# Kernel optimization log

Measured on AMD Instinct MI355X. Metric: run time of the kernel, lower is better.

Reference implementation:

```python
import jax, jax.numpy as jnp
import numpy as np

N_HEAD = 16
D_HEAD = 64
SCALE = 1.0 / D_HEAD ** 0.5


def setup_inputs() -> dict:
    key = jax.random.key(0)
    k1, k2, k3, k4 = jax.random.split(key, 4)
    bsz, qlen, d_embed, d_model = 4, 1024, 768, 1024
    return {
        "word_emb": jax.random.normal(k1, (bsz, qlen, d_embed), dtype=jnp.float32),
        "emb_w": jax.random.normal(k2, (d_embed, d_model), dtype=jnp.float32) * 0.02,
        "emb_b": jnp.zeros((d_model,), dtype=jnp.float32),
        "qkv_w0": jax.random.normal(k3, (d_model, 3 * N_HEAD * D_HEAD), dtype=jnp.float32) * 0.02,
        "qkv_w1": jax.random.normal(k4, (d_model, 3 * N_HEAD * D_HEAD), dtype=jnp.float32) * 0.02,
    }


def _mha(h, qkv_w):
    # h: [qlen, bsz, d_model]
    qlen, bsz, _ = h.shape
    heads = h @ qkv_w  # [qlen, bsz, 3*n_head*d_head]
    head_q, head_k, head_v = jnp.split(heads, 3, axis=-1)
    head_q = head_q.reshape(qlen, bsz, N_HEAD, D_HEAD)
    head_k = head_k.reshape(qlen, bsz, N_HEAD, D_HEAD)
    head_v = head_v.reshape(qlen, bsz, N_HEAD, D_HEAD)
    # explicit score materialization, faithful to the source einsum pattern
    attn_score = jnp.einsum('ibnd,jbnd->ijbn', head_q, head_k) * SCALE
    attn_prob = jax.nn.softmax(attn_score, axis=1)  # softmax over klen (dim=1)
    attn_vec = jnp.einsum('ijbn,jbnd->ibnd', attn_prob, head_v)
    attn_vec = attn_vec.reshape(qlen, bsz, N_HEAD * D_HEAD)
    return attn_vec, attn_prob


def reference(word_emb, emb_w, emb_b, qkv_w0, qkv_w1):
    # word_emb: [bsz, qlen, d_embed] -> [qlen, bsz, d_embed]
    h = jnp.transpose(word_emb, (1, 0, 2))
    h = h @ emb_w + emb_b  # emb_proj since d_embed != d_model
    # NOTE: the source computes pos_emb and word_emb + pos_emb, but then
    # overwrites with core_out = self.drop(word_emb), discarding pos_emb.
    # Dropout is identity in reference (eval) mode, so core_out == h.
    core_out = h
    core_out, attn_maps = _mha(core_out, qkv_w0)
    core_out, attn_maps = _mha(core_out, qkv_w1)
    return core_out, attn_maps
```

## Files before the change

### kernel.cpp

```cpp
#include <hip/hip_runtime.h>

#define LOG2E 1.44269504088896340736f

typedef __attribute__((ext_vector_type(8))) short short8;
typedef __attribute__((ext_vector_type(4))) short short4v;
typedef __attribute__((ext_vector_type(4))) float floatx4;

__device__ __forceinline__ float bf2f(short s) {
    union { float f; unsigned u; } v; v.u = ((unsigned)(unsigned short)s) << 16; return v.f;
}
__device__ __forceinline__ short f2bf(float f) {
    union { float f; unsigned u; } v; v.f = f;
    unsigned u = v.u;
    u += 0x7FFFu + ((u >> 16) & 1u);
    return (short)(u >> 16);
}

__device__ __forceinline__ void gl_lds16(const void* g, void* l) {
    __builtin_amdgcn_global_load_lds((const __attribute__((address_space(1))) void*)g,
                                     (__attribute__((address_space(3))) void*)l, 16, 0, 0);
}

__global__ __launch_bounds__(256) void wcast(const float* __restrict__ W,
                                             short* __restrict__ Wt, int K, int N) {
    __shared__ float tile[64][65];
    int n0 = blockIdx.x * 64, k0 = blockIdx.y * 64;
    int t = threadIdx.x;
    int r = t >> 2, c4 = (t & 3) * 16;
    const float* src = W + (size_t)(k0 + r) * N + n0 + c4;
#pragma unroll
    for (int q = 0; q < 16; ++q) tile[r][c4 + q] = src[q];
    __syncthreads();
    short* dst = Wt + (size_t)(n0 + r) * K + k0 + c4;
    short8 o1, o2;
#pragma unroll
    for (int q = 0; q < 8; ++q) o1[q] = f2bf(tile[c4 + q][r]);
#pragma unroll
    for (int q = 0; q < 8; ++q) o2[q] = f2bf(tile[c4 + 8 + q][r]);
    *(short8*)(dst) = o1;
    *(short8*)(dst + 8) = o2;
}

__global__ __launch_bounds__(256) void a0cast(const float* __restrict__ we,
                                              short* __restrict__ A0) {
    int e = blockIdx.x * 256 + threadIdx.x;
    int m = e / 96, dc = (e % 96) * 8;
    int b = m & 3, s = m >> 2;
    const float* src = we + (size_t)(b * 1024 + s) * 768 + dc;
    short8 o;
#pragma unroll
    for (int q = 0; q < 8; ++q) o[q] = f2bf(src[q]);
    *(short8*)(A0 + (size_t)m * 768 + dc) = o;
}

__global__ __launch_bounds__(256) void gemm_bt(const short* __restrict__ A,
                                               const short* __restrict__ Bt,
                                               short* __restrict__ C,
                                               const float* __restrict__ bias,
                                               int K, int N) {
    __shared__ __align__(16) short sA[128 * 32];
    __shared__ __align__(16) short sB[128 * 32];
    int n0 = blockIdx.x * 128, m0 = blockIdx.y * 128;
    int tid = threadIdx.x;
    int lane = tid & 63, w = tid >> 6;
    int wm = (w >> 1) * 64, wn = (w & 1) * 64;
    int l15 = lane & 15, quad = lane >> 4;
    int srow = lane >> 2, scoff = (lane & 3) * 8;

    floatx4 zero = {0.f, 0.f, 0.f, 0.f};
    floatx4 acc[4][4];
#pragma unroll
    for (int i = 0; i < 4; ++i)
#pragma unroll
        for (int j = 0; j < 4; ++j) acc[i][j] = zero;

    for (int k0 = 0; k0 < K; k0 += 32) {
#pragma unroll
        for (int h = 0; h < 2; ++h) {
            int seg = w * 2 + h;
            int row = seg * 16 + srow;
            gl_lds16(A + (size_t)(m0 + row) * K + k0 + scoff, sA + seg * 512);
            gl_lds16(Bt + (size_t)(n0 + row) * K + k0 + scoff, sB + seg * 512);
        }
        __syncthreads();
        short8 af[4], bfr[4];
#pragma unroll
        for (int i = 0; i < 4; ++i) {
            af[i]  = *(const short8*)(sA + (wm + i * 16 + l15) * 32 + quad * 8);
            bfr[i] = *(const short8*)(sB + (wn + i * 16 + l15) * 32 + quad * 8);
        }
#pragma unroll
        for (int i = 0; i < 4; ++i)
#pragma unroll
            for (int j = 0; j < 4; ++j)
                acc[i][j] = __builtin_amdgcn_mfma_f32_16x16x32_bf16(af[i], bfr[j], acc[i][j], 0, 0, 0);
        __syncthreads();
    }
#pragma unroll
    for (int i = 0; i < 4; ++i)
#pragma unroll
        for (int j = 0; j < 4; ++j) {
            int col = n0 + wn + j * 16 + l15;
            float bv = bias ? bias[col] : 0.f;
#pragma unroll
            for (int r = 0; r < 4; ++r) {
                int row = m0 + wm + i * 16 + quad * 4 + r;
                C[(size_t)row * N + col] = f2bf(acc[i][j][r] + bv);
            }
        }
}

__global__ __launch_bounds__(256) void pack_qkv(const short* __restrict__ heads,
                                                short* __restrict__ Qp,
                                                short* __restrict__ Kp,
                                                short* __restrict__ Vtp) {
    __shared__ short vt[64][72];
    int bn = blockIdx.y;
    int b = bn >> 4, n = bn & 15;
    int j0 = blockIdx.x * 64;
    int t = threadIdx.x;
#pragma unroll
    for (int h = 0; h < 2; ++h) {
        int c = t + h * 256;
        int jj = c >> 3, off = (c & 7) * 8;
        const short* base = heads + (size_t)((j0 + jj) * 4 + b) * 3072 + n * 64 + off;
        short8 qv = *(const short8*)(base);
        short8 kv = *(const short8*)(base + 1024);
        short8 vv = *(const short8*)(base + 2048);
        short8 qs;
#pragma unroll
        for (int e = 0; e < 8; ++e) qs[e] = f2bf(bf2f(qv[e]) * 0.125f);
        *(short8*)(Qp + (size_t)bn * 65536 + (j0 + jj) * 64 + off) = qs;
        *(short8*)(Kp + (size_t)bn * 65536 + (j0 + jj) * 64 + off) = kv;
#pragma unroll
        for (int e = 0; e < 8; ++e) vt[jj][off + e] = vv[e];
    }
    __syncthreads();
#pragma unroll
    for (int h = 0; h < 2; ++h) {
        int c = t + h * 256;
        int d = c >> 3, joff = (c & 7) * 8;
        short8 o;
#pragma unroll
        for (int e = 0; e < 8; ++e) o[e] = vt[joff + e][d];
        *(short8*)(Vtp + (size_t)bn * 65536 + d * 1024 + j0 + joff) = o;
    }
}

template <bool L2>
__global__ __launch_bounds__(64) void fattn(const short* __restrict__ Qp,
                                            const short* __restrict__ Kp,
                                            const short* __restrict__ Vtp,
                                            void* __restrict__ Optr,
                                            float* __restrict__ linv) {
    __shared__ __align__(16) short plds[32 * 32];
    int bn = blockIdx.y, b = bn >> 4, n = bn & 15;
    int i0 = blockIdx.x * 32;
    int lane = threadIdx.x, l15 = lane & 15, quad = lane >> 4;
    const short* Qb = Qp + (size_t)bn * 65536;
    const short* Kb = Kp + (size_t)bn * 65536;
    const short* Vb = Vtp + (size_t)bn * 65536;

    short8 qf[2][2];
#pragma unroll
    for (int ib = 0; ib < 2; ++ib) {
        qf[ib][0] = *(const short8*)(Qb + (i0 + ib * 16 + l15) * 64 + quad * 8);
        qf[ib][1] = *(const short8*)(Qb + (i0 + ib * 16 + l15) * 64 + 32 + quad * 8);
    }
    floatx4 zero = {0.f, 0.f, 0.f, 0.f};
    floatx4 o[2][4];
#pragma unroll
    for (int ib = 0; ib < 2; ++ib)
#pragma unroll
        for (int tt = 0; tt < 4; ++tt) o[ib][tt] = zero;
    float lsum[2] = {0.f, 0.f};

    for (int j0 = 0; j0 < 1024; j0 += 32) {
#pragma unroll
        for (int jb = 0; jb < 2; ++jb) {
            const short* kr = Kb + (j0 + jb * 16 + l15) * 64 + quad * 8;
            short8 kf0 = *(const short8*)(kr);
            short8 kf1 = *(const short8*)(kr + 32);
#pragma unroll
            for (int ib = 0; ib < 2; ++ib) {
                floatx4 s = zero;
                s = __builtin_amdgcn_mfma_f32_16x16x32_bf16(kf0, qf[ib][0], s, 0, 0, 0);
                s = __builtin_amdgcn_mfma_f32_16x16x32_bf16(kf1, qf[ib][1], s, 0, 0, 0);
                short4v pk;
                float ls = 0.f;
#pragma unroll
                for (int r = 0; r < 4; ++r) {
                    float p = __builtin_amdgcn_exp2f(s[r] * LOG2E);
                    ls += p;
                    pk[r] = f2bf(p);
                }
                lsum[ib] += ls;
                *(short4v*)(plds + (ib * 16 + l15) * 32 + jb * 16 + quad * 4) = pk;
            }
        }
        __syncthreads();
        short8 pa[2];
        pa[0] = *(const short8*)(plds + l15 * 32 + quad * 8);
        pa[1] = *(const short8*)(plds + (16 + l15) * 32 + quad * 8);
#pragma unroll
        for (int tt = 0; tt < 4; ++tt) {
            short8 vf = *(const short8*)(Vb + (tt * 16 + l15) * 1024 + j0 + quad * 8);
#pragma unroll
            for (int ib = 0; ib < 2; ++ib)
                o[ib][tt] = __builtin_amdgcn_mfma_f32_16x16x32_bf16(pa[ib], vf, o[ib][tt], 0, 0, 0);
        }
        __syncthreads();
    }
    float rinv[2];
#pragma unroll
    for (int ib = 0; ib < 2; ++ib) {
        float t = lsum[ib];
        t += __shfl_xor(t, 16);
        t += __shfl_xor(t, 32);
        rinv[ib] = 1.f / t;
    }
    if (L2 && quad == 0) {
        linv[bn * 1024 + i0 + l15] = rinv[0];
        linv[bn * 1024 + i0 + 16 + l15] = rinv[1];
    }
    float rn[2][4];
#pragma unroll
    for (int ib = 0; ib < 2; ++ib)
#pragma unroll
        for (int r = 0; r < 4; ++r)
            rn[ib][r] = __shfl(rinv[ib], quad * 4 + r);
#pragma unroll
    for (int ib = 0; ib < 2; ++ib)
#pragma unroll
        for (int tt = 0; tt < 4; ++tt)
#pragma unroll
            for (int r = 0; r < 4; ++r) {
                float val = o[ib][tt][r] * rn[ib][r];
                int row = i0 + ib * 16 + quad * 4 + r;
                int col = n * 64 + tt * 16 + l15;
                size_t idx = (size_t)(row * 4 + b) * 1024 + col;
                if (L2) ((float*)Optr)[idx] = val;
                else    ((short*)Optr)[idx] = f2bf(val);
            }
}

__global__ __launch_bounds__(256) void pfin(const short* __restrict__ Qp,
                                            const short* __restrict__ Kp,
                                            const float* __restrict__ linv,
                                            float* __restrict__ Pout) {
    __shared__ short sP[64 * 512];
    int j0 = blockIdx.x * 32, i0 = blockIdx.y * 16;
    int tid = threadIdx.x, wv = tid >> 6, lane = tid & 63;
    int l15 = lane & 15, quad = lane >> 4;
    floatx4 zero = {0.f, 0.f, 0.f, 0.f};
    for (int bi = 0; bi < 16; ++bi) {
        int bn = wv * 16 + bi;
        const short* Qb = Qp + (size_t)bn * 65536;
        const short* Kb = Kp + (size_t)bn * 65536;
        short8 qf0 = *(const short8*)(Qb + (i0 + l15) * 64 + quad * 8);
        short8 qf1 = *(const short8*)(Qb + (i0 + l15) * 64 + 32 + quad * 8);
        float li = linv[bn * 1024 + i0 + l15];
#pragma unroll
        for (int jb = 0; jb < 2; ++jb) {
            const short* kr = Kb + (j0 + jb * 16 + l15) * 64 + quad * 8;
            short8 kf0 = *(const short8*)(kr);
            short8 kf1 = *(const short8*)(kr + 32);
            floatx4 s = zero;
            s = __builtin_amdgcn_mfma_f32_16x16x32_bf16(kf0, qf0, s, 0, 0, 0);
            s = __builtin_amdgcn_mfma_f32_16x16x32_bf16(kf1, qf1, s, 0, 0, 0);
            short4v pk;
#pragma unroll
            for (int r = 0; r < 4; ++r)
                pk[r] = f2bf(__builtin_amdgcn_exp2f(s[r] * LOG2E) * li);
            *(short4v*)(sP + bn * 512 + l15 * 32 + jb * 16 + quad * 4) = pk;
        }
    }
    __syncthreads();
    int ii = tid >> 4, q = tid & 15;
    float* dst = Pout + (size_t)(i0 + ii) * 65536 + j0 * 64 + q * 128;
#pragma unroll
    for (int e4 = 0; e4 < 32; ++e4) {
        int pos = q * 128 + e4 * 4;
        int jj = pos >> 6, bnb = pos & 63;
        float4 v;
        v.x = bf2f(sP[(bnb + 0) * 512 + ii * 32 + jj]);
        v.y = bf2f(sP[(bnb + 1) * 512 + ii * 32 + jj]);
        v.z = bf2f(sP[(bnb + 2) * 512 + ii * 32 + jj]);
        v.w = bf2f(sP[(bnb + 3) * 512 + ii * 32 + jj]);
        *(float4*)(dst + e4 * 4) = v;
    }
}

extern "C" void kernel_launch(void* const* d_in, const int* in_sizes, int n_in,
                              void* d_out, int out_size, void* d_ws, size_t ws_size,
                              hipStream_t stream) {
    const float* word_emb = (const float*)d_in[0];
    const float* emb_w    = (const float*)d_in[1];
    const float* emb_b    = (const float*)d_in[2];
    const float* qkv_w0   = (const float*)d_in[3];
    const float* qkv_w1   = (const float*)d_in[4];
    float* out0 = (float*)d_out;
    float* out1 = out0 + 4194304;

    char* ws = (char*)d_ws;
    short* A0    = (short*)(ws);
    short* WtE   = (short*)(ws + 6291456);
    short* Wt0   = (short*)(ws + 7864320);
    short* Wt1   = (short*)(ws + 14155776);
    short* hbuf  = (short*)(ws + 20447232);
    short* h2    = (short*)(ws + 28835840);
    short* heads = (short*)(ws + 37224448);
    short* Qp    = (short*)(ws + 62390272);
    short* Kp    = (short*)(ws + 70778880);
    short* Vtp   = (short*)(ws + 79167488);
    float* linv  = (float*)(ws + 87556096);

    wcast<<<dim3(16, 12), 256, 0, stream>>>(emb_w, WtE, 768, 1024);
    wcast<<<dim3(48, 16), 256, 0, stream>>>(qkv_w0, Wt0, 1024, 3072);
    wcast<<<dim3(48, 16), 256, 0, stream>>>(qkv_w1, Wt1, 1024, 3072);
    a0cast<<<1536, 256, 0, stream>>>(word_emb, A0);

    gemm_bt<<<dim3(8, 32), 256, 0, stream>>>(A0, WtE, hbuf, emb_b, 768, 1024);
    gemm_bt<<<dim3(24, 32), 256, 0, stream>>>(hbuf, Wt0, heads, nullptr, 1024, 3072);
    pack_qkv<<<dim3(16, 64), 256, 0, stream>>>(heads, Qp, Kp, Vtp);
    fattn<false><<<dim3(32, 64), 64, 0, stream>>>(Qp, Kp, Vtp, (void*)h2, nullptr);
    gemm_bt<<<dim3(24, 32), 256, 0, stream>>>(h2, Wt1, heads, nullptr, 1024, 3072);
    pack_qkv<<<dim3(16, 64), 256, 0, stream>>>(heads, Qp, Kp, Vtp);
    fattn<true><<<dim3(32, 64), 64, 0, stream>>>(Qp, Kp, Vtp, (void*)out0, linv);
    pfin<<<dim3(32, 64), 256, 0, stream>>>(Qp, Kp, linv, out1);
}
```

Baseline: 686.2 us.

## Merge prep casts, widen GEMM K-tile with swizzled LDS, vectorize epilogue stores

Merges the three weight-transpose casts and the activation cast into one prep kernel, which cuts launch count. The GEMM now stages a 64-wide K tile per barrier through an XOR-swizzled LDS layout to avoid bank conflicts. It also swaps the MFMA operands so each lane holds four consecutive columns, which lets the GEMM and attention epilogues write packed 4-element vectors instead of scalar strided stores. This doubles the GEMM's LDS footprint, which could lower occupancy, and the operand swap changes the accumulator layout everywhere it is consumed.

```diff
diff --git a/kernel.cpp b/kernel.cpp
--- a/kernel.cpp
+++ b/kernel.cpp
@@ -21,11 +21,10 @@
                                      (__attribute__((address_space(3))) void*)l, 16, 0, 0);
 }
 
-__global__ __launch_bounds__(256) void wcast(const float* __restrict__ W,
-                                             short* __restrict__ Wt, int K, int N) {
+__device__ __forceinline__ void wcast_tile(const float* __restrict__ W,
+                                           short* __restrict__ Wt, int K, int N,
+                                           int n0, int k0, int t) {
     __shared__ float tile[64][65];
-    int n0 = blockIdx.x * 64, k0 = blockIdx.y * 64;
-    int t = threadIdx.x;
     int r = t >> 2, c4 = (t & 3) * 16;
     const float* src = W + (size_t)(k0 + r) * N + n0 + c4;
 #pragma unroll
@@ -41,16 +40,34 @@
     *(short8*)(dst + 8) = o2;
 }
 
-__global__ __launch_bounds__(256) void a0cast(const float* __restrict__ we,
-                                              short* __restrict__ A0) {
-    int e = blockIdx.x * 256 + threadIdx.x;
-    int m = e / 96, dc = (e % 96) * 8;
-    int b = m & 3, s = m >> 2;
-    const float* src = we + (size_t)(b * 1024 + s) * 768 + dc;
-    short8 o;
-#pragma unroll
-    for (int q = 0; q < 8; ++q) o[q] = f2bf(src[q]);
-    *(short8*)(A0 + (size_t)m * 768 + dc) = o;
+__global__ __launch_bounds__(256) void prep(const float* __restrict__ we,
+                                            const float* __restrict__ emb_w,
+                                            const float* __restrict__ qkv_w0,
+                                            const float* __restrict__ qkv_w1,
+                                            short* __restrict__ A0,
+                                            short* __restrict__ WtE,
+                                            short* __restrict__ Wt0,
+                                            short* __restrict__ Wt1) {
+    int bid = blockIdx.x, t = threadIdx.x;
+    if (bid < 1536) {
+        int e = bid * 256 + t;
+        int m = e / 96, dc = (e % 96) * 8;
+        int b = m & 3, s = m >> 2;
+        const float* src = we + (size_t)(b * 1024 + s) * 768 + dc;
+        short8 o;
+#pragma unroll
+        for (int q = 0; q < 8; ++q) o[q] = f2bf(src[q]);
+        *(short8*)(A0 + (size_t)m * 768 + dc) = o;
+    } else if (bid < 1728) {
+        int tt = bid - 1536;
+        wcast_tile(emb_w, WtE, 768, 1024, (tt & 15) * 64, (tt >> 4) * 64, t);
+    } else if (bid < 2496) {
+        int tt = bid - 1728;
+        wcast_tile(qkv_w0, Wt0, 1024, 3072, (tt % 48) * 64, (tt / 48) * 64, t);
+    } else {
+        int tt = bid - 2496;
+        wcast_tile(qkv_w1, Wt1, 1024, 3072, (tt % 48) * 64, (tt / 48) * 64, t);
+    }
 }
 
 __global__ __launch_bounds__(256) void gemm_bt(const short* __restrict__ A,
@@ -58,14 +75,14 @@
                                                short* __restrict__ C,
                                                const float* __restrict__ bias,
                                                int K, int N) {
-    __shared__ __align__(16) short sA[128 * 32];
-    __shared__ __align__(16) short sB[128 * 32];
+    __shared__ __align__(16) short sA[128 * 64];
+    __shared__ __align__(16) short sB[128 * 64];
     int n0 = blockIdx.x * 128, m0 = blockIdx.y * 128;
     int tid = threadIdx.x;
     int lane = tid & 63, w = tid >> 6;
     int wm = (w >> 1) * 64, wn = (w & 1) * 64;
     int l15 = lane & 15, quad = lane >> 4;
-    int srow = lane >> 2, scoff = (lane & 3) * 8;
+    int lrow = lane >> 3, lchunk = (lane & 7) ^ lrow;
 
     floatx4 zero = {0.f, 0.f, 0.f, 0.f};
     floatx4 acc[4][4];
@@ -74,40 +91,47 @@
 #pragma unroll
         for (int j = 0; j < 4; ++j) acc[i][j] = zero;
 
-    for (int k0 = 0; k0 < K; k0 += 32) {
+    for (int k0 = 0; k0 < K; k0 += 64) {
+#pragma unroll
+        for (int c = 0; c < 4; ++c) {
+            int r0 = w * 32 + c * 8;
+            int row = r0 + lrow;
+            gl_lds16(A + (size_t)(m0 + row) * K + k0 + lchunk * 8, sA + r0 * 64);
+            gl_lds16(Bt + (size_t)(n0 + row) * K + k0 + lchunk * 8, sB + r0 * 64);
+        }
+        __syncthreads();
 #pragma unroll
         for (int h = 0; h < 2; ++h) {
-            int seg = w * 2 + h;
-            int row = seg * 16 + srow;
-            gl_lds16(A + (size_t)(m0 + row) * K + k0 + scoff, sA + seg * 512);
-            gl_lds16(Bt + (size_t)(n0 + row) * K + k0 + scoff, sB + seg * 512);
+            int sw = ((h * 4 + quad) ^ (l15 & 7)) * 8;
+            short8 af[4], bfr[4];
+#pragma unroll
+            for (int i = 0; i < 4; ++i) {
+                af[i]  = *(const short8*)(sA + (wm + i * 16 + l15) * 64 + sw);
+                bfr[i] = *(const short8*)(sB + (wn + i * 16 + l15) * 64 + sw);
+            }
+#pragma unroll
+            for (int i = 0; i < 4; ++i)
+#pragma unroll
+                for (int j = 0; j < 4; ++j)
+                    acc[i][j] = __builtin_amdgcn_mfma_f32_16x16x32_bf16(bfr[j], af[i], acc[i][j], 0, 0, 0);
         }
         __syncthreads();
-        short8 af[4], bfr[4];
-#pragma unroll
-        for (int i = 0; i < 4; ++i) {
-            af[i]  = *(const short8*)(sA + (wm + i * 16 + l15) * 32 + quad * 8);
-            bfr[i] = *(const short8*)(sB + (wn + i * 16 + l15) * 32 + quad * 8);
-        }
-#pragma unroll
-        for (int i = 0; i < 4; ++i)
-#pragma unroll
-            for (int j = 0; j < 4; ++j)
-                acc[i][j] = __builtin_amdgcn_mfma_f32_16x16x32_bf16(af[i], bfr[j], acc[i][j], 0, 0, 0);
-        __syncthreads();
-    }
-#pragma unroll
-    for (int i = 0; i < 4; ++i)
+    }
+#pragma unroll
+    for (int i = 0; i < 4; ++i) {
+        int row = m0 + wm + i * 16 + l15;
 #pragma unroll
         for (int j = 0; j < 4; ++j) {
-            int col = n0 + wn + j * 16 + l15;
-            float bv = bias ? bias[col] : 0.f;
-#pragma unroll
-            for (int r = 0; r < 4; ++r) {
-                int row = m0 + wm + i * 16 + quad * 4 + r;
-                C[(size_t)row * N + col] = f2bf(acc[i][j][r] + bv);
-            }
-        }
+            int colb = n0 + wn + j * 16 + quad * 4;
+            float4 bv = bias ? *(const float4*)(bias + colb) : float4{0.f, 0.f, 0.f, 0.f};
+            short4v st;
+            st[0] = f2bf(acc[i][j][0] + bv.x);
+            st[1] = f2bf(acc[i][j][1] + bv.y);
+            st[2] = f2bf(acc[i][j][2] + bv.z);
+            st[3] = f2bf(acc[i][j][3] + bv.w);
+            *(short4v*)(C + (size_t)row * N + colb) = st;
+        }
+    }
 }
 
 __global__ __launch_bounds__(256) void pack_qkv(const short* __restrict__ heads,
@@ -207,7 +231,7 @@
             short8 vf = *(const short8*)(Vb + (tt * 16 + l15) * 1024 + j0 + quad * 8);
 #pragma unroll
             for (int ib = 0; ib < 2; ++ib)
-                o[ib][tt] = __builtin_amdgcn_mfma_f32_16x16x32_bf16(pa[ib], vf, o[ib][tt], 0, 0, 0);
+                o[ib][tt] = __builtin_amdgcn_mfma_f32_16x16x32_bf16(vf, pa[ib], o[ib][tt], 0, 0, 0);
         }
         __syncthreads();
     }
@@ -223,25 +247,27 @@
         linv[bn * 1024 + i0 + l15] = rinv[0];
         linv[bn * 1024 + i0 + 16 + l15] = rinv[1];
     }
-    float rn[2][4];
 #pragma unroll
     for (int ib = 0; ib < 2; ++ib)
 #pragma unroll
-        for (int r = 0; r < 4; ++r)
-            rn[ib][r] = __shfl(rinv[ib], quad * 4 + r);
-#pragma unroll
-    for (int ib = 0; ib < 2; ++ib)
-#pragma unroll
-        for (int tt = 0; tt < 4; ++tt)
-#pragma unroll
-            for (int r = 0; r < 4; ++r) {
-                float val = o[ib][tt][r] * rn[ib][r];
-                int row = i0 + ib * 16 + quad * 4 + r;
-                int col = n * 64 + tt * 16 + l15;
-                size_t idx = (size_t)(row * 4 + b) * 1024 + col;
-                if (L2) ((float*)Optr)[idx] = val;
-                else    ((short*)Optr)[idx] = f2bf(val);
+        for (int tt = 0; tt < 4; ++tt) {
+            int row = i0 + ib * 16 + l15;
+            int colb = n * 64 + tt * 16 + quad * 4;
+            size_t idx = (size_t)(row * 4 + b) * 1024 + colb;
+            if (L2) {
+                float4 v;
+                v.x = o[ib][tt][0] * rinv[ib];
+                v.y = o[ib][tt][1] * rinv[ib];
+                v.z = o[ib][tt][2] * rinv[ib];
+                v.w = o[ib][tt][3] * rinv[ib];
+                *(float4*)((float*)Optr + idx) = v;
+            } else {
+                short4v st;
+#pragma unroll
+                for (int r = 0; r < 4; ++r) st[r] = f2bf(o[ib][tt][r] * rinv[ib]);
+                *(short4v*)((short*)Optr + idx) = st;
             }
+        }
 }
 
 __global__ __launch_bounds__(256) void pfin(const short* __restrict__ Qp,
@@ -315,10 +341,7 @@
     short* Vtp   = (short*)(ws + 79167488);
     float* linv  = (float*)(ws + 87556096);
 
-    wcast<<<dim3(16, 12), 256, 0, stream>>>(emb_w, WtE, 768, 1024);
-    wcast<<<dim3(48, 16), 256, 0, stream>>>(qkv_w0, Wt0, 1024, 3072);
-    wcast<<<dim3(48, 16), 256, 0, stream>>>(qkv_w1, Wt1, 1024, 3072);
-    a0cast<<<1536, 256, 0, stream>>>(word_emb, A0);
+    prep<<<3264, 256, 0, stream>>>(word_emb, emb_w, qkv_w0, qkv_w1, A0, WtE, Wt0, Wt1);
 
     gemm_bt<<<dim3(8, 32), 256, 0, stream>>>(A0, WtE, hbuf, emb_b, 768, 1024);
     gemm_bt<<<dim3(24, 32), 256, 0, stream>>>(hbuf, Wt0, heads, nullptr, 1024, 3072);
```

After: 658.6 us. 1.04x faster.
